# Kernel tuning notes

Measured on AMD Instinct MI355X. Metric: run time of the kernel, lower is better.

Reference implementation:

```python
import jax, jax.numpy as jnp
import numpy as np

PATCH_SIZE = 16
STRIDE = 16


def setup_inputs() -> dict:
    key = jax.random.key(0)
    k1, k2 = jax.random.split(key)
    x = jax.random.normal(k1, (64, 64, 8192), dtype=jnp.float32)
    mask = jax.random.randint(k2, (64, 8192), 0, 2, dtype=jnp.int32)
    return {"x": x, "mask": mask}


def reference(x, mask):
    B, C, S = x.shape
    P, St = PATCH_SIZE, STRIDE
    n_patches = 1 + (S - P) // St
    # window gather indices: [n_patches, P]
    idx = jnp.arange(n_patches)[:, None] * St + jnp.arange(P)[None, :]
    # x[:, :, idx] -> [B, C, n_patches, P]; torch stacks on dim=1 -> [B, n_patches, C, P]
    patches = jnp.transpose(x[:, :, idx], (0, 2, 1, 3)).reshape(B, n_patches, C * P)
    # per-patch valid ratio over the window, thresholded at 0.5 -> float mask [B, n_patches]
    valid_ratio = jnp.mean(mask[:, idx].astype(jnp.float32), axis=-1)
    padding_mask = (valid_ratio >= 0.5).astype(jnp.float32)
    return patches, padding_mask
```

## Files before the change

kernel.cpp:

```cpp
#include <hip/hip_runtime.h>


constexpr int Bb  = 64;
constexpr int Cc  = 64;
constexpr int Ss  = 8192;
constexpr int NP  = 512;
constexpr size_t PATCH_ELEMS = (size_t)Bb * NP * Cc * 16;

__global__ __launch_bounds__(256) void ts_patcher_kernel(
    const float* __restrict__ x,
    const int*   __restrict__ mask,
    float*       __restrict__ out)
{
    const int t    = threadIdx.x;
    const int lane = t & 63;
    const int w    = t >> 6;
    const int blk  = blockIdx.x;
    const int b    = blk >> 7;
    const int p    = (blk & 127) * 4 + w;

    const float* xb = x + (size_t)b * Cc * Ss;
    float* orow = out + ((size_t)(b * NP + p) * (Cc * 16));

    const int cbase = lane >> 2;
    const int j     = (lane & 3) * 4;
    const int xoff  = p * 16 + j;

#pragma unroll
    for (int k = 0; k < 4; ++k) {
        const int c = k * 16 + cbase;
        const float4 v = *(const float4*)(xb + (size_t)c * Ss + xoff);
        *(float4*)(orow + k * 256 + lane * 4) = v;
    }

    if (lane == 0) {
        const int4* m = (const int4*)(mask + (size_t)b * Ss + p * 16);
        int4 a = m[0], d = m[1], e = m[2], f = m[3];
        int s = a.x + a.y + a.z + a.w
              + d.x + d.y + d.z + d.w
              + e.x + e.y + e.z + e.w
              + f.x + f.y + f.z + f.w;
        out[PATCH_ELEMS + (size_t)b * NP + p] = (s >= 8) ? 1.0f : 0.0f;
    }
}

extern "C" void kernel_launch(void* const* d_in, const int* in_sizes, int n_in,
                              void* d_out, int out_size, void* d_ws, size_t ws_size,
                              hipStream_t stream) {
    const float* x    = (const float*)d_in[0];
    const int*   mask = (const int*)d_in[1];
    float*       out  = (float*)d_out;

    const int blocks = Bb * (NP / 4);
    ts_patcher_kernel<<<blocks, 256, 0, stream>>>(x, mask, out);
}
```

Before: 235.5 us.

## Stage 8-patch input tiles through LDS for coalesced 512B row reads

Each block now handles 8 consecutive patches. It loads a 64-channel by 128-float tile with fully coalesced 512-byte row reads into padded shared memory, then writes the patches out contiguously from LDS. This replaces the earlier pattern of 64-byte segments per channel row, aiming at better DRAM read efficiency. In exchange it adds LDS traffic, a barrier and fewer blocks.

After: 228.2 us. 3.1% less time.

```diff
diff --git a/kernel.cpp b/kernel.cpp
--- a/kernel.cpp
+++ b/kernel.cpp
@@ -5,6 +5,9 @@
 constexpr int Cc  = 64;
 constexpr int Ss  = 8192;
 constexpr int NP  = 512;
+constexpr int PT  = 8;
+constexpr int ROWF = PT * 16;
+constexpr int LSTRIDE = ROWF + 4;
 constexpr size_t PATCH_ELEMS = (size_t)Bb * NP * Cc * 16;
 
 __global__ __launch_bounds__(256) void ts_patcher_kernel(
@@ -12,28 +15,41 @@
     const int*   __restrict__ mask,
     float*       __restrict__ out)
 {
-    const int t    = threadIdx.x;
-    const int lane = t & 63;
-    const int w    = t >> 6;
-    const int blk  = blockIdx.x;
-    const int b    = blk >> 7;
-    const int p    = (blk & 127) * 4 + w;
+    __shared__ float lds[Cc * LSTRIDE];
 
-    const float* xb = x + (size_t)b * Cc * Ss;
-    float* orow = out + ((size_t)(b * NP + p) * (Cc * 16));
+    const int t   = threadIdx.x;
+    const int blk = blockIdx.x;
+    const int b   = blk >> 6;
+    const int P0  = (blk & 63) * PT;
 
-    const int cbase = lane >> 2;
-    const int j     = (lane & 3) * 4;
-    const int xoff  = p * 16 + j;
+    const float* xb = x + (size_t)b * Cc * Ss + P0 * 16;
 
+    {
+        const int c0  = t >> 5;
+        const int col = (t & 31) * 4;
 #pragma unroll
-    for (int k = 0; k < 4; ++k) {
-        const int c = k * 16 + cbase;
-        const float4 v = *(const float4*)(xb + (size_t)c * Ss + xoff);
-        *(float4*)(orow + k * 256 + lane * 4) = v;
+        for (int i = 0; i < 8; ++i) {
+            const int c = i * 8 + c0;
+            const float4 v = *(const float4*)(xb + (size_t)c * Ss + col);
+            *(float4*)(&lds[c * LSTRIDE + col]) = v;
+        }
     }
 
-    if (lane == 0) {
+    __syncthreads();
+
+    {
+        float* otile = out + ((size_t)(b * NP + P0) * (Cc * 16));
+        const int c = t >> 2;
+        const int j = (t & 3) * 4;
+#pragma unroll
+        for (int i = 0; i < 8; ++i) {
+            const float4 v = *(const float4*)(&lds[c * LSTRIDE + i * 16 + j]);
+            *(float4*)(otile + (size_t)i * 1024 + t * 4) = v;
+        }
+    }
+
+    if (t < PT) {
+        const int p = P0 + t;
         const int4* m = (const int4*)(mask + (size_t)b * Ss + p * 16);
         int4 a = m[0], d = m[1], e = m[2], f = m[3];
         int s = a.x + a.y + a.z + a.w
@@ -51,6 +67,6 @@
     const int*   mask = (const int*)d_in[1];
     float*       out  = (float*)d_out;
 
-    const int blocks = Bb * (NP / 4);
+    const int blocks = Bb * (NP / PT);
     ts_patcher_kernel<<<blocks, 256, 0, stream>>>(x, mask, out);
 }
```
